# Optimization experiments

Measured on AMD Instinct MI355X. Metric: run time of the kernel, lower is better.

## Reference

```python
import jax, jax.numpy as jnp
import numpy as np

B, T, D = 64, 1024, 512
H, O = 512, 128
HALF = D // 2
ALPHA_M = 0.8


def setup_inputs() -> dict:
    key = jax.random.key(0)
    ks = jax.random.split(key, 6)
    s_in = 1.0 / np.sqrt(HALF)
    s_h = 1.0 / np.sqrt(H)
    return {
        "x": jax.random.normal(ks[0], (B, T, D), dtype=jnp.float32),
        "w1": jax.random.uniform(ks[1], (H, HALF), jnp.float32, -s_in, s_in),
        "b1": jnp.zeros((H,), jnp.float32),
        "tau1": jnp.full((H,), 3.0, jnp.float32),
        "w2": jax.random.uniform(ks[2], (H, HALF), jnp.float32, -s_in, s_in),
        "b2": jnp.zeros((H,), jnp.float32),
        "tau2": jnp.full((H,), 0.5, jnp.float32),
        "wo": jax.random.uniform(ks[3], (O, H), jnp.float32, -s_h, s_h),
        "bo": jnp.zeros((O,), jnp.float32),
    }


def reference(x, w1, b1, tau1, w2, b2, tau2, wo, bo):
    # Hoist the per-timestep branch Linears into two batched GEMMs.
    d1_in = jnp.einsum("bti,hi->tbh", x[:, :, :HALF], w1) + b1  # [T,B,H]
    d2_in = jnp.einsum("bti,hi->tbh", x[:, :, HALF:], w2) + b2  # [T,B,H]

    a1 = jax.nn.sigmoid(tau1)  # [H]
    a2 = jax.nn.sigmoid(tau2)  # [H]

    def step(carry, ins):
        d1, d2, mem = carry
        i1, i2 = ins
        d1 = a1 * d1 + (1.0 - a1) * i1
        d2 = a2 * d2 + (1.0 - a2) * i2
        mem = ALPHA_M * mem + (1.0 - ALPHA_M) * (d1 + d2)
        return (d1, d2, mem), mem

    z = jnp.zeros((x.shape[0], tau1.shape[0]), x.dtype)
    _, mems = jax.lax.scan(step, (z, z, z), (d1_in, d2_in))  # mems: [T,B,H]

    # Output projection + sigmoid, vectorized over all timesteps.
    out = jax.nn.sigmoid(jnp.einsum("tbh,oh->bto", mems, wo) + bo)  # [B,T,O]
    return out
```

## Files before the change

kernel.cpp:

```cpp
#include <hip/hip_runtime.h>


#define B_    64
#define T_    1024
#define D_    512
#define H_    512
#define O_    128
#define HALF_ 256
#define CLEN  32
#define NC    32

typedef __attribute__((ext_vector_type(4))) float        f32x4;
typedef __attribute__((ext_vector_type(2))) float        f32x2;
typedef __attribute__((ext_vector_type(8))) short        s16x8;
typedef __attribute__((ext_vector_type(4))) unsigned int u32x4;

__device__ __forceinline__ unsigned short f2bf(float f) {
    unsigned u = __float_as_uint(f);
    return (unsigned short)((u + 0x7fffu + ((u >> 16) & 1u)) >> 16);
}
__device__ __forceinline__ unsigned packbf(float a, float b) {
    return (unsigned)f2bf(a) | ((unsigned)f2bf(b) << 16);
}
__device__ __forceinline__ float bflo(unsigned u) { return __uint_as_float(u << 16); }
__device__ __forceinline__ float bfhi(unsigned u) { return __uint_as_float(u & 0xffff0000u); }
__device__ __forceinline__ float sigf(float x) { return 1.f / (1.f + __expf(-x)); }
__device__ __forceinline__ float pw32(float a) {
    float t = a * a; t *= t; t *= t; t *= t; t *= t; return t;
}

typedef const __attribute__((address_space(1))) unsigned int gu32;
typedef __attribute__((address_space(3))) unsigned int      lu32;
__device__ __forceinline__ void gl_lds16(const void* g, void* l) {
    __builtin_amdgcn_global_load_lds((gu32*)g, (lu32*)l, 16, 0, 0);
}

__global__ __launch_bounds__(256) void cast_kernel(const float* __restrict__ x,
                                                   unsigned int* __restrict__ xb) {
    size_t i = ((size_t)blockIdx.x * 256 + threadIdx.x) * 8;
    f32x4 a = *(const f32x4*)(x + i);
    f32x4 b = *(const f32x4*)(x + i + 4);
    u32x4 p;
    p.x = packbf(a.x, a.y); p.y = packbf(a.z, a.w);
    p.z = packbf(b.x, b.y); p.w = packbf(b.z, b.w);
    *(u32x4*)(xb + i / 2) = p;
}

__global__ __launch_bounds__(256, 2) void gemm1_kernel(
    const unsigned short* __restrict__ xb, const float* __restrict__ w1,
    const float* __restrict__ w2, unsigned short* __restrict__ din1,
    unsigned short* __restrict__ din2)
{
    __shared__ short As[128 * 64];
    __shared__ short Bs[128 * 64];

    const int nt = blockIdx.x, mt = blockIdx.y, br = blockIdx.z;
    const float* w = br ? w2 : w1;
    unsigned short* dout = br ? din2 : din1;
    const int koff = br * HALF_;

    const int tid = threadIdx.x, l = tid & 63, wv = tid >> 6;
    const int ln = l & 15, qd = l >> 4;
    const int wm = (wv & 1) << 6, wn = (wv >> 1) << 6;

    f32x4 acc[4][4] = {};

    const unsigned short* abase = xb + (size_t)(mt * 128) * D_ + koff;
    const float* wbase = w + (size_t)(nt * 128) * HALF_;

    for (int kt = 0; kt < HALF_; kt += 64) {
        #pragma unroll
        for (int i = 0; i < 4; ++i) {
            int ch = wv * 4 + i;
            int r  = ch * 8 + (l >> 3);
            int kbl = (l & 7) ^ (r & 7);
            gl_lds16(abase + (size_t)r * D_ + kt + kbl * 8, &As[ch * 512 + l * 8]);
        }
        #pragma unroll
        for (int i = 0; i < 4; ++i) {
            int gi = i * 256 + tid;
            int r = gi >> 3, kbp = gi & 7, kbl = kbp ^ (r & 7);
            const float* src = wbase + (size_t)r * HALF_ + kt + kbl * 8;
            f32x4 b0 = *(const f32x4*)src;
            f32x4 b1v = *(const f32x4*)(src + 4);
            u32x4 pb;
            pb.x = packbf(b0.x, b0.y); pb.y = packbf(b0.z, b0.w);
            pb.z = packbf(b1v.x, b1v.y); pb.w = packbf(b1v.z, b1v.w);
            *(u32x4*)&Bs[r * 64 + kbp * 8] = pb;
        }
        __syncthreads();
        #pragma unroll
        for (int ks = 0; ks < 64; ks += 32) {
            s16x8 af[4], bfv[4];
            #pragma unroll
            for (int i = 0; i < 4; ++i) {
                int r = wm + i * 16 + ln;
                int kbp = ((ks >> 3) + qd) ^ (r & 7);
                af[i] = *(const s16x8*)&As[r * 64 + kbp * 8];
            }
            #pragma unroll
            for (int j = 0; j < 4; ++j) {
                int r = wn + j * 16 + ln;
                int kbp = ((ks >> 3) + qd) ^ (r & 7);
                bfv[j] = *(const s16x8*)&Bs[r * 64 + kbp * 8];
            }
            #pragma unroll
            for (int i = 0; i < 4; ++i)
                #pragma unroll
                for (int j = 0; j < 4; ++j)
                    acc[i][j] = __builtin_amdgcn_mfma_f32_16x16x32_bf16(
                        af[i], bfv[j], acc[i][j], 0, 0, 0);
        }
        __syncthreads();
    }

    unsigned short* orow = dout + (size_t)(mt * 128 + wm + qd * 4) * H_ + nt * 128 + wn + ln;
    #pragma unroll
    for (int i = 0; i < 4; ++i)
        #pragma unroll
        for (int j = 0; j < 4; ++j)
            #pragma unroll
            for (int r = 0; r < 4; ++r)
                orow[(size_t)(i * 16 + r) * H_ + j * 16] = f2bf(acc[i][j][r]);
}

__global__ __launch_bounds__(256) void scanA_kernel(
    unsigned int* __restrict__ m1,
    const unsigned int* __restrict__ p2,
    const float* __restrict__ b1, const float* __restrict__ tau1,
    const float* __restrict__ b2, const float* __restrict__ tau2,
    float* __restrict__ Sd1, float* __restrict__ Sd2, float* __restrict__ Sm)
{
    const int h2 = threadIdx.x;
    const int c = blockIdx.x & (NC - 1);
    const int b = blockIdx.x >> 5;
    const int h0 = h2 << 1;

    const float a1a = sigf(tau1[h0]), a1b = sigf(tau1[h0 + 1]);
    const float a2a = sigf(tau2[h0]), a2b = sigf(tau2[h0 + 1]);
    const float o1a = 1.f - a1a, o1b = 1.f - a1b;
    const float o2a = 1.f - a2a, o2b = 1.f - a2b;
    const float bb1a = b1[h0], bb1b = b1[h0 + 1];
    const float bb2a = b2[h0], bb2b = b2[h0 + 1];

    const size_t base = ((size_t)b * T_ + c * CLEN) * (H_ / 2) + h2;
    float d1a = 0.f, d1b = 0.f, d2a = 0.f, d2b = 0.f, ma = 0.f, mb = 0.f;

    #pragma unroll 8
    for (int k = 0; k < CLEN; ++k) {
        unsigned u1 = m1[base + (size_t)k * (H_ / 2)];
        unsigned u2 = p2[base + (size_t)k * (H_ / 2)];
        float i1a = bflo(u1) + bb1a, i1b = bfhi(u1) + bb1b;
        float i2a = bflo(u2) + bb2a, i2b = bfhi(u2) + bb2b;
        d1a = a1a * d1a + o1a * i1a;  d1b = a1b * d1b + o1b * i1b;
        d2a = a2a * d2a + o2a * i2a;  d2b = a2b * d2b + o2b * i2b;
        ma = 0.8f * ma + 0.2f * (d1a + d2a);
        mb = 0.8f * mb + 0.2f * (d1b + d2b);
        m1[base + (size_t)k * (H_ / 2)] = packbf(ma, mb);
    }

    const size_t si = ((size_t)c * B_ + b) * H_ + h0;
    f32x2 v;
    v.x = d1a; v.y = d1b; *(f32x2*)&Sd1[si] = v;
    v.x = d2a; v.y = d2b; *(f32x2*)&Sd2[si] = v;
    v.x = ma;  v.y = mb;  *(f32x2*)&Sm[si]  = v;
}

__global__ __launch_bounds__(128) void scanB_kernel(
    const float* __restrict__ Sd1, const float* __restrict__ Sd2,
    const float* __restrict__ Sm,
    const float* __restrict__ tau1, const float* __restrict__ tau2,
    float* __restrict__ D1, float* __restrict__ D2, float* __restrict__ DM)
{
    const int g = blockIdx.x * 128 + threadIdx.x;
    const int h2 = g & 255, b = g >> 8, h0 = h2 << 1;

    const float a1a = sigf(tau1[h0]), a1b = sigf(tau1[h0 + 1]);
    const float a2a = sigf(tau2[h0]), a2b = sigf(tau2[h0 + 1]);
    const float amL = pw32(0.8f);
    const float a1La = pw32(a1a), a1Lb = pw32(a1b);
    const float a2La = pw32(a2a), a2Lb = pw32(a2b);

    float dn;
    dn = 0.8f - a1a; if (fabsf(dn) < 1e-6f) dn = (dn < 0.f ? -1e-6f : 1e-6f);
    const float c1a = 0.2f * a1a / dn;
    dn = 0.8f - a1b; if (fabsf(dn) < 1e-6f) dn = (dn < 0.f ? -1e-6f : 1e-6f);
    const float c1b = 0.2f * a1b / dn;
    dn = 0.8f - a2a; if (fabsf(dn) < 1e-6f) dn = (dn < 0.f ? -1e-6f : 1e-6f);
    const float c2a = 0.2f * a2a / dn;
    dn = 0.8f - a2b; if (fabsf(dn) < 1e-6f) dn = (dn < 0.f ? -1e-6f : 1e-6f);
    const float c2b = 0.2f * a2b / dn;

    const float g1La = c1a * (amL - a1La), g1Lb = c1b * (amL - a1Lb);
    const float g2La = c2a * (amL - a2La), g2Lb = c2b * (amL - a2Lb);

    float D1a = 0.f, D1b = 0.f, D2a = 0.f, D2b = 0.f, Ma = 0.f, Mb = 0.f;
    for (int c = 0; c < NC; ++c) {
        const size_t si = ((size_t)c * B_ + b) * H_ + h0;
        if (c) {
            f32x2 v;
            v.x = D1a; v.y = D1b; *(f32x2*)&D1[si] = v;
            v.x = D2a; v.y = D2b; *(f32x2*)&D2[si] = v;
            v.x = Ma;  v.y = Mb;  *(f32x2*)&DM[si] = v;
        }
        f32x2 s1 = *(const f32x2*)&Sd1[si];
        f32x2 s2 = *(const f32x2*)&Sd2[si];
        f32x2 sm = *(const f32x2*)&Sm[si];
        float nMa = amL * Ma + D1a * g1La + D2a * g2La + sm.x;
        float nMb = amL * Mb + D1b * g1Lb + D2b * g2Lb + sm.y;
        D1a = a1La * D1a + s1.x;  D1b = a1Lb * D1b + s1.y;
        D2a = a2La * D2a + s2.x;  D2b = a2Lb * D2b + s2.y;
        Ma = nMa;  Mb = nMb;
    }
}

__global__ __launch_bounds__(256) void scanC_kernel(
    unsigned int* __restrict__ mems,
    const float* __restrict__ tau1, const float* __restrict__ tau2,
    const float* __restrict__ D1, const float* __restrict__ D2,
    const float* __restrict__ DM)
{
    const int h2 = threadIdx.x;
    const int c = blockIdx.x % (NC - 1) + 1;
    const int b = blockIdx.x / (NC - 1);
    const int h0 = h2 << 1;

    const size_t si = ((size_t)c * B_ + b) * H_ + h0;
    f32x2 d1 = *(const f32x2*)&D1[si];
    f32x2 d2 = *(const f32x2*)&D2[si];
    f32x2 mm = *(const f32x2*)&DM[si];

    const float a1a = sigf(tau1[h0]), a1b = sigf(tau1[h0 + 1]);
    const float a2a = sigf(tau2[h0]), a2b = sigf(tau2[h0 + 1]);
    float dn;
    dn = 0.8f - a1a; if (fabsf(dn) < 1e-6f) dn = (dn < 0.f ? -1e-6f : 1e-6f);
    const float c1a = 0.2f * a1a / dn;
    dn = 0.8f - a1b; if (fabsf(dn) < 1e-6f) dn = (dn < 0.f ? -1e-6f : 1e-6f);
    const float c1b = 0.2f * a1b / dn;
    dn = 0.8f - a2a; if (fabsf(dn) < 1e-6f) dn = (dn < 0.f ? -1e-6f : 1e-6f);
    const float c2a = 0.2f * a2a / dn;
    dn = 0.8f - a2b; if (fabsf(dn) < 1e-6f) dn = (dn < 0.f ? -1e-6f : 1e-6f);
    const float c2b = 0.2f * a2b / dn;

    float pm = 1.f, p1a = 1.f, p1b = 1.f, p2a = 1.f, p2b = 1.f;
    const size_t base = ((size_t)b * T_ + c * CLEN) * (H_ / 2) + h2;

    #pragma unroll 8
    for (int k = 0; k < CLEN; ++k) {
        pm *= 0.8f; p1a *= a1a; p1b *= a1b; p2a *= a2a; p2b *= a2b;
        float g1a = c1a * (pm - p1a), g2a = c2a * (pm - p2a);
        float g1b = c1b * (pm - p1b), g2b = c2b * (pm - p2b);
        unsigned u = mems[base + (size_t)k * (H_ / 2)];
        float va = bflo(u) + d1.x * g1a + d2.x * g2a + mm.x * pm;
        float vb = bfhi(u) + d1.y * g1b + d2.y * g2b + mm.y * pm;
        mems[base + (size_t)k * (H_ / 2)] = packbf(va, vb);
    }
}

__global__ __launch_bounds__(256, 2) void gemm2_kernel(
    const unsigned short* __restrict__ mems, const float* __restrict__ wo,
    const float* __restrict__ bo, float* __restrict__ out)
{
    __shared__ short As[128 * 64];
    __shared__ short Bs[128 * 64];

    const int mt = blockIdx.x;
    const int tid = threadIdx.x, l = tid & 63, wv = tid >> 6;
    const int ln = l & 15, qd = l >> 4;
    const int wm = (wv & 1) << 6, wn = (wv >> 1) << 6;

    f32x4 acc[4][4] = {};
    const unsigned short* abase = mems + (size_t)(mt * 128) * H_;

    for (int kt = 0; kt < H_; kt += 64) {
        #pragma unroll
        for (int i = 0; i < 4; ++i) {
            int ch = wv * 4 + i;
            int r  = ch * 8 + (l >> 3);
            int kbl = (l & 7) ^ (r & 7);
            gl_lds16(abase + (size_t)r * H_ + kt + kbl * 8, &As[ch * 512 + l * 8]);
        }
        #pragma unroll
        for (int i = 0; i < 4; ++i) {
            int gi = i * 256 + tid;
            int r = gi >> 3, kbp = gi & 7, kbl = kbp ^ (r & 7);
            const float* src = wo + (size_t)r * H_ + kt + kbl * 8;
            f32x4 b0 = *(const f32x4*)src;
            f32x4 b1v = *(const f32x4*)(src + 4);
            u32x4 pb;
            pb.x = packbf(b0.x, b0.y); pb.y = packbf(b0.z, b0.w);
            pb.z = packbf(b1v.x, b1v.y); pb.w = packbf(b1v.z, b1v.w);
            *(u32x4*)&Bs[r * 64 + kbp * 8] = pb;
        }
        __syncthreads();
        #pragma unroll
        for (int ks = 0; ks < 64; ks += 32) {
            s16x8 af[4], bfv[4];
            #pragma unroll
            for (int i = 0; i < 4; ++i) {
                int r = wm + i * 16 + ln;
                int kbp = ((ks >> 3) + qd) ^ (r & 7);
                af[i] = *(const s16x8*)&As[r * 64 + kbp * 8];
            }
            #pragma unroll
            for (int j = 0; j < 4; ++j) {
                int r = wn + j * 16 + ln;
                int kbp = ((ks >> 3) + qd) ^ (r & 7);
                bfv[j] = *(const s16x8*)&Bs[r * 64 + kbp * 8];
            }
            #pragma unroll
            for (int i = 0; i < 4; ++i)
                #pragma unroll
                for (int j = 0; j < 4; ++j)
                    acc[i][j] = __builtin_amdgcn_mfma_f32_16x16x32_bf16(
                        af[i], bfv[j], acc[i][j], 0, 0, 0);
        }
        __syncthreads();
    }

    float bov[4];
    #pragma unroll
    for (int j = 0; j < 4; ++j) bov[j] = bo[wn + j * 16 + ln];

    float* orow = out + (size_t)(mt * 128 + wm + qd * 4) * O_ + wn + ln;
    #pragma unroll
    for (int i = 0; i < 4; ++i)
        #pragma unroll
        for (int j = 0; j < 4; ++j)
            #pragma unroll
            for (int r = 0; r < 4; ++r) {
                float v = acc[i][j][r] + bov[j];
                orow[(size_t)(i * 16 + r) * O_ + j * 16] = 1.f / (1.f + __expf(-v));
            }
}

extern "C" void kernel_launch(void* const* d_in, const int* in_sizes, int n_in,
                              void* d_out, int out_size, void* d_ws, size_t ws_size,
                              hipStream_t stream) {
    const float* x    = (const float*)d_in[0];
    const float* w1   = (const float*)d_in[1];
    const float* b1   = (const float*)d_in[2];
    const float* tau1 = (const float*)d_in[3];
    const float* w2   = (const float*)d_in[4];
    const float* b2   = (const float*)d_in[5];
    const float* tau2 = (const float*)d_in[6];
    const float* wo   = (const float*)d_in[7];
    const float* bo   = (const float*)d_in[8];
    float* out = (float*)d_out;

    char* w = (char*)d_ws;
    unsigned short* xb   = (unsigned short*)(w);
    unsigned short* din1 = (unsigned short*)(w + (size_t)64 * 1024 * 1024);
    unsigned short* din2 = (unsigned short*)(w + (size_t)128 * 1024 * 1024);
    float* Sd1 = (float*)w;
    float* Sd2 = Sd1 + (1u << 20);
    float* Sm  = Sd1 + (2u << 20);
    float* D1  = Sd1 + (3u << 20);
    float* D2  = Sd1 + (4u << 20);
    float* DM  = Sd1 + (5u << 20);

    cast_kernel<<<dim3(16384), 256, 0, stream>>>(x, (unsigned int*)xb);
    gemm1_kernel<<<dim3(4, 512, 2), 256, 0, stream>>>(xb, w1, w2, din1, din2);
    scanA_kernel<<<dim3(B_ * NC), 256, 0, stream>>>((unsigned int*)din1,
                                                    (const unsigned int*)din2,
                                                    b1, tau1, b2, tau2, Sd1, Sd2, Sm);
    scanB_kernel<<<dim3(128), 128, 0, stream>>>(Sd1, Sd2, Sm, tau1, tau2, D1, D2, DM);
    scanC_kernel<<<dim3(B_ * (NC - 1)), 256, 0, stream>>>((unsigned int*)din1,
                                                          tau1, tau2, D1, D2, DM);
    gemm2_kernel<<<dim3(512), 256, 0, stream>>>(din1, wo, bo, out);
}
```

Baseline: 366.2 us.

## Fuse chunk-local scan into GEMM1 epilogue and carry fixup into GEMM2 loader

```diff
diff --git a/kernel.cpp b/kernel.cpp
--- a/kernel.cpp
+++ b/kernel.cpp
@@ -25,6 +25,10 @@
 __device__ __forceinline__ float bflo(unsigned u) { return __uint_as_float(u << 16); }
 __device__ __forceinline__ float bfhi(unsigned u) { return __uint_as_float(u & 0xffff0000u); }
 __device__ __forceinline__ float sigf(float x) { return 1.f / (1.f + __expf(-x)); }
+__device__ __forceinline__ float guard(float dn) {
+    if (fabsf(dn) < 1e-6f) dn = (dn < 0.f ? -1e-6f : 1e-6f);
+    return dn;
+}
 __device__ __forceinline__ float pw32(float a) {
     float t = a * a; t *= t; t *= t; t *= t; t *= t; return t;
 }
@@ -33,6 +37,22 @@
 typedef __attribute__((address_space(3))) unsigned int      lu32;
 __device__ __forceinline__ void gl_lds16(const void* g, void* l) {
     __builtin_amdgcn_global_load_lds((gu32*)g, (lu32*)l, 16, 0, 0);
+}
+
+__global__ __launch_bounds__(256) void gtab_kernel(
+    const float* __restrict__ tau1, const float* __restrict__ tau2,
+    float* __restrict__ G1, float* __restrict__ G2)
+{
+    const int h = blockIdx.x * 256 + threadIdx.x;
+    const float a1 = sigf(tau1[h]), a2 = sigf(tau2[h]);
+    const float c1 = 0.2f * a1 / guard(0.8f - a1);
+    const float c2 = 0.2f * a2 / guard(0.8f - a2);
+    float pm = 1.f, p1 = 1.f, p2 = 1.f;
+    for (int k = 0; k < CLEN; ++k) {
+        pm *= 0.8f; p1 *= a1; p2 *= a2;
+        G1[k * H_ + h] = c1 * (pm - p1);
+        G2[k * H_ + h] = c2 * (pm - p2);
+    }
 }
 
 __global__ __launch_bounds__(256) void cast_kernel(const float* __restrict__ x,
@@ -46,120 +66,124 @@
     *(u32x4*)(xb + i / 2) = p;
 }
 
-__global__ __launch_bounds__(256, 2) void gemm1_kernel(
+__global__ __launch_bounds__(256, 2) void gemm1f_kernel(
     const unsigned short* __restrict__ xb, const float* __restrict__ w1,
-    const float* __restrict__ w2, unsigned short* __restrict__ din1,
-    unsigned short* __restrict__ din2)
+    const float* __restrict__ w2,
+    const float* __restrict__ b1, const float* __restrict__ tau1,
+    const float* __restrict__ b2, const float* __restrict__ tau2,
+    unsigned int* __restrict__ mems,
+    float* __restrict__ Sd1, float* __restrict__ Sd2, float* __restrict__ Sm)
 {
-    __shared__ short As[128 * 64];
-    __shared__ short Bs[128 * 64];
-
-    const int nt = blockIdx.x, mt = blockIdx.y, br = blockIdx.z;
-    const float* w = br ? w2 : w1;
-    unsigned short* dout = br ? din2 : din1;
-    const int koff = br * HALF_;
+    __shared__ short smem[32768];
+    short* As  = smem;
+    short* Bs  = smem + 8192;
+    short* d1L = smem + 16384;
+    short* d2L = smem;
+
+    const int nt = blockIdx.x;
+    const int mt = blockIdx.y;
+    const int b  = mt >> 3;
+    const int t0 = (mt & 7) << 7;
 
     const int tid = threadIdx.x, l = tid & 63, wv = tid >> 6;
     const int ln = l & 15, qd = l >> 4;
     const int wm = (wv & 1) << 6, wn = (wv >> 1) << 6;
 
-    f32x4 acc[4][4] = {};
-
-    const unsigned short* abase = xb + (size_t)(mt * 128) * D_ + koff;
-    const float* wbase = w + (size_t)(nt * 128) * HALF_;
-
-    for (int kt = 0; kt < HALF_; kt += 64) {
-        #pragma unroll
-        for (int i = 0; i < 4; ++i) {
-            int ch = wv * 4 + i;
-            int r  = ch * 8 + (l >> 3);
-            int kbl = (l & 7) ^ (r & 7);
-            gl_lds16(abase + (size_t)r * D_ + kt + kbl * 8, &As[ch * 512 + l * 8]);
+    for (int br = 0; br < 2; ++br) {
+        const float* w = br ? w2 : w1;
+        const unsigned short* abase = xb + (size_t)(mt * 128) * D_ + br * HALF_;
+        const float* wbase = w + (size_t)(nt * 128) * HALF_;
+
+        f32x4 acc[4][4] = {};
+
+        for (int kt = 0; kt < HALF_; kt += 64) {
+            #pragma unroll
+            for (int i = 0; i < 4; ++i) {
+                int ch = wv * 4 + i;
+                int r  = ch * 8 + (l >> 3);
+                int kbl = (l & 7) ^ (r & 7);
+                gl_lds16(abase + (size_t)r * D_ + kt + kbl * 8, &As[ch * 512 + l * 8]);
+            }
+            #pragma unroll
+            for (int i = 0; i < 4; ++i) {
+                int gi = i * 256 + tid;
+                int r = gi >> 3, kbp = gi & 7, kbl = kbp ^ (r & 7);
+                const float* src = wbase + (size_t)r * HALF_ + kt + kbl * 8;
+                f32x4 b0 = *(const f32x4*)src;
+                f32x4 b1v = *(const f32x4*)(src + 4);
+                u32x4 pb;
+                pb.x = packbf(b0.x, b0.y); pb.y = packbf(b0.z, b0.w);
+                pb.z = packbf(b1v.x, b1v.y); pb.w = packbf(b1v.z, b1v.w);
+                *(u32x4*)&Bs[r * 64 + kbp * 8] = pb;
+            }
+            __syncthreads();
+            #pragma unroll
+            for (int ks = 0; ks < 64; ks += 32) {
+                s16x8 af[4], bfv[4];
+                #pragma unroll
+                for (int i = 0; i < 4; ++i) {
+                    int r = wm + i * 16 + ln;
+                    int kbp = ((ks >> 3) + qd) ^ (r & 7);
+                    af[i] = *(const s16x8*)&As[r * 64 + kbp * 8];
+                }
+                #pragma unroll
+                for (int j = 0; j < 4; ++j) {
+                    int r = wn + j * 16 + ln;
+                    int kbp = ((ks >> 3) + qd) ^ (r & 7);
+                    bfv[j] = *(const s16x8*)&Bs[r * 64 + kbp * 8];
+                }
+                #pragma unroll
+                for (int i = 0; i < 4; ++i)
+                    #pragma unroll
+                    for (int j = 0; j < 4; ++j)
+                        acc[i][j] = __builtin_amdgcn_mfma_f32_16x16x32_bf16(
+                            af[i], bfv[j], acc[i][j], 0, 0, 0);
+            }
+            __syncthreads();
         }
-        #pragma unroll
-        for (int i = 0; i < 4; ++i) {
-            int gi = i * 256 + tid;
-            int r = gi >> 3, kbp = gi & 7, kbl = kbp ^ (r & 7);
-            const float* src = wbase + (size_t)r * HALF_ + kt + kbl * 8;
-            f32x4 b0 = *(const f32x4*)src;
-            f32x4 b1v = *(const f32x4*)(src + 4);
-            u32x4 pb;
-            pb.x = packbf(b0.x, b0.y); pb.y = packbf(b0.z, b0.w);
-            pb.z = packbf(b1v.x, b1v.y); pb.w = packbf(b1v.z, b1v.w);
-            *(u32x4*)&Bs[r * 64 + kbp * 8] = pb;
-        }
-        __syncthreads();
-        #pragma unroll
-        for (int ks = 0; ks < 64; ks += 32) {
-            s16x8 af[4], bfv[4];
-            #pragma unroll
-            for (int i = 0; i < 4; ++i) {
-                int r = wm + i * 16 + ln;
-                int kbp = ((ks >> 3) + qd) ^ (r & 7);
-                af[i] = *(const s16x8*)&As[r * 64 + kbp * 8];
-            }
-            #pragma unroll
-            for (int j = 0; j < 4; ++j) {
-                int r = wn + j * 16 + ln;
-                int kbp = ((ks >> 3) + qd) ^ (r & 7);
-                bfv[j] = *(const s16x8*)&Bs[r * 64 + kbp * 8];
-            }
-            #pragma unroll
-            for (int i = 0; i < 4; ++i)
-                #pragma unroll
-                for (int j = 0; j < 4; ++j)
-                    acc[i][j] = __builtin_amdgcn_mfma_f32_16x16x32_bf16(
-                        af[i], bfv[j], acc[i][j], 0, 0, 0);
-        }
-        __syncthreads();
-    }
-
-    unsigned short* orow = dout + (size_t)(mt * 128 + wm + qd * 4) * H_ + nt * 128 + wn + ln;
-    #pragma unroll
-    for (int i = 0; i < 4; ++i)
-        #pragma unroll
-        for (int j = 0; j < 4; ++j)
-            #pragma unroll
-            for (int r = 0; r < 4; ++r)
-                orow[(size_t)(i * 16 + r) * H_ + j * 16] = f2bf(acc[i][j][r]);
-}
-
-__global__ __launch_bounds__(256) void scanA_kernel(
-    unsigned int* __restrict__ m1,
-    const unsigned int* __restrict__ p2,
-    const float* __restrict__ b1, const float* __restrict__ tau1,
-    const float* __restrict__ b2, const float* __restrict__ tau2,
-    float* __restrict__ Sd1, float* __restrict__ Sd2, float* __restrict__ Sm)
-{
-    const int h2 = threadIdx.x;
-    const int c = blockIdx.x & (NC - 1);
-    const int b = blockIdx.x >> 5;
-    const int h0 = h2 << 1;
-
-    const float a1a = sigf(tau1[h0]), a1b = sigf(tau1[h0 + 1]);
-    const float a2a = sigf(tau2[h0]), a2b = sigf(tau2[h0 + 1]);
+
+        short* dL = br ? d2L : d1L;
+        #pragma unroll
+        for (int i = 0; i < 4; ++i)
+            #pragma unroll
+            for (int j = 0; j < 4; ++j)
+                #pragma unroll
+                for (int r = 0; r < 4; ++r)
+                    dL[(wm + i * 16 + qd * 4 + r) * 128 + wn + j * 16 + ln] =
+                        (short)f2bf(acc[i][j][r]);
+    }
+    __syncthreads();
+
+    const int cl  = tid >> 6;
+    const int h2l = tid & 63;
+    const int hl0 = h2l << 1;
+    const int hg0 = nt * 128 + hl0;
+    const int cg  = ((mt & 7) << 2) + cl;
+
+    const float a1a = sigf(tau1[hg0]), a1b = sigf(tau1[hg0 + 1]);
+    const float a2a = sigf(tau2[hg0]), a2b = sigf(tau2[hg0 + 1]);
     const float o1a = 1.f - a1a, o1b = 1.f - a1b;
     const float o2a = 1.f - a2a, o2b = 1.f - a2b;
-    const float bb1a = b1[h0], bb1b = b1[h0 + 1];
-    const float bb2a = b2[h0], bb2b = b2[h0 + 1];
-
-    const size_t base = ((size_t)b * T_ + c * CLEN) * (H_ / 2) + h2;
+    const float bb1a = b1[hg0], bb1b = b1[hg0 + 1];
+    const float bb2a = b2[hg0], bb2b = b2[hg0 + 1];
+
     float d1a = 0.f, d1b = 0.f, d2a = 0.f, d2b = 0.f, ma = 0.f, mb = 0.f;
+    const size_t mrow = (size_t)(b * T_ + t0 + cl * CLEN) * (H_ / 2) + nt * 64 + h2l;
 
     #pragma unroll 8
     for (int k = 0; k < CLEN; ++k) {
-        unsigned u1 = m1[base + (size_t)k * (H_ / 2)];
-        unsigned u2 = p2[base + (size_t)k * (H_ / 2)];
+        unsigned u1 = *(const unsigned*)&d1L[(cl * CLEN + k) * 128 + hl0];
+        unsigned u2 = *(const unsigned*)&d2L[(cl * CLEN + k) * 128 + hl0];
         float i1a = bflo(u1) + bb1a, i1b = bfhi(u1) + bb1b;
         float i2a = bflo(u2) + bb2a, i2b = bfhi(u2) + bb2b;
         d1a = a1a * d1a + o1a * i1a;  d1b = a1b * d1b + o1b * i1b;
         d2a = a2a * d2a + o2a * i2a;  d2b = a2b * d2b + o2b * i2b;
         ma = 0.8f * ma + 0.2f * (d1a + d2a);
         mb = 0.8f * mb + 0.2f * (d1b + d2b);
-        m1[base + (size_t)k * (H_ / 2)] = packbf(ma, mb);
-    }
-
-    const size_t si = ((size_t)c * B_ + b) * H_ + h0;
+        mems[mrow + (size_t)k * (H_ / 2)] = packbf(ma, mb);
+    }
+
+    const size_t si = (size_t)(cg * B_ + b) * H_ + hg0;
     f32x2 v;
     v.x = d1a; v.y = d1b; *(f32x2*)&Sd1[si] = v;
     v.x = d2a; v.y = d2b; *(f32x2*)&Sd2[si] = v;
@@ -181,28 +205,21 @@
     const float a1La = pw32(a1a), a1Lb = pw32(a1b);
     const float a2La = pw32(a2a), a2Lb = pw32(a2b);
 
-    float dn;
-    dn = 0.8f - a1a; if (fabsf(dn) < 1e-6f) dn = (dn < 0.f ? -1e-6f : 1e-6f);
-    const float c1a = 0.2f * a1a / dn;
-    dn = 0.8f - a1b; if (fabsf(dn) < 1e-6f) dn = (dn < 0.f ? -1e-6f : 1e-6f);
-    const float c1b = 0.2f * a1b / dn;
-    dn = 0.8f - a2a; if (fabsf(dn) < 1e-6f) dn = (dn < 0.f ? -1e-6f : 1e-6f);
-    const float c2a = 0.2f * a2a / dn;
-    dn = 0.8f - a2b; if (fabsf(dn) < 1e-6f) dn = (dn < 0.f ? -1e-6f : 1e-6f);
-    const float c2b = 0.2f * a2b / dn;
+    const float c1a = 0.2f * a1a / guard(0.8f - a1a);
+    const float c1b = 0.2f * a1b / guard(0.8f - a1b);
+    const float c2a = 0.2f * a2a / guard(0.8f - a2a);
+    const float c2b = 0.2f * a2b / guard(0.8f - a2b);
 
     const float g1La = c1a * (amL - a1La), g1Lb = c1b * (amL - a1Lb);
     const float g2La = c2a * (amL - a2La), g2Lb = c2b * (amL - a2Lb);
 
     float D1a = 0.f, D1b = 0.f, D2a = 0.f, D2b = 0.f, Ma = 0.f, Mb = 0.f;
     for (int c = 0; c < NC; ++c) {
-        const size_t si = ((size_t)c * B_ + b) * H_ + h0;
-        if (c) {
-            f32x2 v;
-            v.x = D1a; v.y = D1b; *(f32x2*)&D1[si] = v;
-            v.x = D2a; v.y = D2b; *(f32x2*)&D2[si] = v;
-            v.x = Ma;  v.y = Mb;  *(f32x2*)&DM[si] = v;
-        }
+        const size_t si = (size_t)(c * B_ + b) * H_ + h0;
+        f32x2 v;
+        v.x = D1a; v.y = D1b; *(f32x2*)&D1[si] = v;
+        v.x = D2a; v.y = D2b; *(f32x2*)&D2[si] = v;
+        v.x = Ma;  v.y = Mb;  *(f32x2*)&DM[si] = v;
         f32x2 s1 = *(const f32x2*)&Sd1[si];
         f32x2 s2 = *(const f32x2*)&Sd2[si];
         f32x2 sm = *(const f32x2*)&Sm[si];
@@ -214,71 +231,60 @@
     }
 }
 
-__global__ __launch_bounds__(256) void scanC_kernel(
-    unsigned int* __restrict__ mems,
-    const float* __restrict__ tau1, const float* __restrict__ tau2,
+__global__ __launch_bounds__(256, 2) void gemm2f_kernel(
+    const unsigned short* __restrict__ mems, const float* __restrict__ wo,
+    const float* __restrict__ bo,
+    const float* __restrict__ G1, const float* __restrict__ G2,
     const float* __restrict__ D1, const float* __restrict__ D2,
-    const float* __restrict__ DM)
-{
-    const int h2 = threadIdx.x;
-    const int c = blockIdx.x % (NC - 1) + 1;
-    const int b = blockIdx.x / (NC - 1);
-    const int h0 = h2 << 1;
-
-    const size_t si = ((size_t)c * B_ + b) * H_ + h0;
-    f32x2 d1 = *(const f32x2*)&D1[si];
-    f32x2 d2 = *(const f32x2*)&D2[si];
-    f32x2 mm = *(const f32x2*)&DM[si];
-
-    const float a1a = sigf(tau1[h0]), a1b = sigf(tau1[h0 + 1]);
-    const float a2a = sigf(tau2[h0]), a2b = sigf(tau2[h0 + 1]);
-    float dn;
-    dn = 0.8f - a1a; if (fabsf(dn) < 1e-6f) dn = (dn < 0.f ? -1e-6f : 1e-6f);
-    const float c1a = 0.2f * a1a / dn;
-    dn = 0.8f - a1b; if (fabsf(dn) < 1e-6f) dn = (dn < 0.f ? -1e-6f : 1e-6f);
-    const float c1b = 0.2f * a1b / dn;
-    dn = 0.8f - a2a; if (fabsf(dn) < 1e-6f) dn = (dn < 0.f ? -1e-6f : 1e-6f);
-    const float c2a = 0.2f * a2a / dn;
-    dn = 0.8f - a2b; if (fabsf(dn) < 1e-6f) dn = (dn < 0.f ? -1e-6f : 1e-6f);
-    const float c2b = 0.2f * a2b / dn;
-
-    float pm = 1.f, p1a = 1.f, p1b = 1.f, p2a = 1.f, p2b = 1.f;
-    const size_t base = ((size_t)b * T_ + c * CLEN) * (H_ / 2) + h2;
-
-    #pragma unroll 8
-    for (int k = 0; k < CLEN; ++k) {
-        pm *= 0.8f; p1a *= a1a; p1b *= a1b; p2a *= a2a; p2b *= a2b;
-        float g1a = c1a * (pm - p1a), g2a = c2a * (pm - p2a);
-        float g1b = c1b * (pm - p1b), g2b = c2b * (pm - p2b);
-        unsigned u = mems[base + (size_t)k * (H_ / 2)];
-        float va = bflo(u) + d1.x * g1a + d2.x * g2a + mm.x * pm;
-        float vb = bfhi(u) + d1.y * g1b + d2.y * g2b + mm.y * pm;
-        mems[base + (size_t)k * (H_ / 2)] = packbf(va, vb);
-    }
-}
-
-__global__ __launch_bounds__(256, 2) void gemm2_kernel(
-    const unsigned short* __restrict__ mems, const float* __restrict__ wo,
-    const float* __restrict__ bo, float* __restrict__ out)
+    const float* __restrict__ DM, float* __restrict__ out)
 {
     __shared__ short As[128 * 64];
     __shared__ short Bs[128 * 64];
+    __shared__ float PMl[CLEN];
 
     const int mt = blockIdx.x;
+    const int b = mt >> 3, c0 = (mt & 7) << 2;
     const int tid = threadIdx.x, l = tid & 63, wv = tid >> 6;
     const int ln = l & 15, qd = l >> 4;
     const int wm = (wv & 1) << 6, wn = (wv >> 1) << 6;
 
+    if (tid < CLEN) {
+        float pm = 1.f;
+        for (int k = 0; k <= tid; ++k) pm *= 0.8f;
+        PMl[tid] = pm;
+    }
+    __syncthreads();
+
     f32x4 acc[4][4] = {};
     const unsigned short* abase = mems + (size_t)(mt * 128) * H_;
 
     for (int kt = 0; kt < H_; kt += 64) {
         #pragma unroll
         for (int i = 0; i < 4; ++i) {
-            int ch = wv * 4 + i;
-            int r  = ch * 8 + (l >> 3);
-            int kbl = (l & 7) ^ (r & 7);
-            gl_lds16(abase + (size_t)r * H_ + kt + kbl * 8, &As[ch * 512 + l * 8]);
+            int gi = i * 256 + tid;
+            int r = gi >> 3, kbp = gi & 7, kbl = kbp ^ (r & 7);
+            int h0 = kt + kbl * 8;
+            int k = r & 31, c = c0 + (r >> 5);
+            size_t dbase = (size_t)(c * B_ + b) * H_ + h0;
+            f32x4 d1a = *(const f32x4*)&D1[dbase], d1b = *(const f32x4*)&D1[dbase + 4];
+            f32x4 d2a = *(const f32x4*)&D2[dbase], d2b = *(const f32x4*)&D2[dbase + 4];
+            f32x4 dma = *(const f32x4*)&DM[dbase], dmb = *(const f32x4*)&DM[dbase + 4];
+            f32x4 g1a = *(const f32x4*)&G1[k * H_ + h0], g1b = *(const f32x4*)&G1[k * H_ + h0 + 4];
+            f32x4 g2a = *(const f32x4*)&G2[k * H_ + h0], g2b = *(const f32x4*)&G2[k * H_ + h0 + 4];
+            float pm = PMl[k];
+            u32x4 mv = *(const u32x4*)(abase + (size_t)r * H_ + h0);
+            float v0 = bflo(mv.x) + d1a.x * g1a.x + d2a.x * g2a.x + dma.x * pm;
+            float v1 = bfhi(mv.x) + d1a.y * g1a.y + d2a.y * g2a.y + dma.y * pm;
+            float v2 = bflo(mv.y) + d1a.z * g1a.z + d2a.z * g2a.z + dma.z * pm;
+            float v3 = bfhi(mv.y) + d1a.w * g1a.w + d2a.w * g2a.w + dma.w * pm;
+            float v4 = bflo(mv.z) + d1b.x * g1b.x + d2b.x * g2b.x + dmb.x * pm;
+            float v5 = bfhi(mv.z) + d1b.y * g1b.y + d2b.y * g2b.y + dmb.y * pm;
+            float v6 = bflo(mv.w) + d1b.z * g1b.z + d2b.z * g2b.z + dmb.z * pm;
+            float v7 = bfhi(mv.w) + d1b.w * g1b.w + d2b.w * g2b.w + dmb.w * pm;
+            u32x4 p;
+            p.x = packbf(v0, v1); p.y = packbf(v2, v3);
+            p.z = packbf(v4, v5); p.w = packbf(v6, v7);
+            *(u32x4*)&As[r * 64 + kbp * 8] = p;
         }
         #pragma unroll
         for (int i = 0; i < 4; ++i) {
@@ -350,22 +356,21 @@
 
     char* w = (char*)d_ws;
     unsigned short* xb   = (unsigned short*)(w);
-    unsigned short* din1 = (unsigned short*)(w + (size_t)64 * 1024 * 1024);
-    unsigned short* din2 = (unsigned short*)(w + (size_t)128 * 1024 * 1024);
-    float* Sd1 = (float*)w;
+    unsigned int*   mems = (unsigned int*)(w + (size_t)64 * 1024 * 1024);
+    float* Sd1 = (float*)(w + (size_t)128 * 1024 * 1024);
     float* Sd2 = Sd1 + (1u << 20);
     float* Sm  = Sd1 + (2u << 20);
     float* D1  = Sd1 + (3u << 20);
     float* D2  = Sd1 + (4u << 20);
     float* DM  = Sd1 + (5u << 20);
-
+    float* G1  = Sd1 + (6u << 20);
+    float* G2  = G1 + CLEN * H_;
+
+    gtab_kernel<<<dim3(2), 256, 0, stream>>>(tau1, tau2, G1, G2);
     cast_kernel<<<dim3(16384), 256, 0, stream>>>(x, (unsigned int*)xb);
-    gemm1_kernel<<<dim3(4, 512, 2), 256, 0, stream>>>(xb, w1, w2, din1, din2);
-    scanA_kernel<<<dim3(B_ * NC), 256, 0, stream>>>((unsigned int*)din1,
-                                                    (const unsigned int*)din2,
-                                                    b1, tau1, b2, tau2, Sd1, Sd2, Sm);
+    gemm1f_kernel<<<dim3(4, 512), 256, 0, stream>>>(xb, w1, w2, b1, tau1, b2, tau2,
+                                                    mems, Sd1, Sd2, Sm);
     scanB_kernel<<<dim3(128), 128, 0, stream>>>(Sd1, Sd2, Sm, tau1, tau2, D1, D2, DM);
-    scanC_kernel<<<dim3(B_ * (NC - 1)), 256, 0, stream>>>((unsigned int*)din1,
-                                                          tau1, tau2, D1, D2, DM);
-    gemm2_kernel<<<dim3(512), 256, 0, stream>>>(din1, wo, bo, out);
-}
+    gemm2f_kernel<<<dim3(512), 256, 0, stream>>>((const unsigned short*)mems, wo, bo,
+                                                 G1, G2, D1, D2, DM, out);
+}
```

Measured after the change: 364.8 us. Within noise of the previous version (-0.4%).
